# Kernel tuning notes

Hardware: AMD Instinct MI355X
Metric: run time of the kernel (lower is better)

## Reference

```python
import jax, jax.numpy as jnp
import numpy as np
from itertools import product

PBC_RADIUS = 1
# (K,3) integer image offsets, K = 27 for radius 1
_OFFSETS = jnp.asarray(np.array(list(product(range(-PBC_RADIUS, PBC_RADIUS + 1), repeat=3)), dtype=np.float32))


def _nan0(x):
    return jnp.nan_to_num(x, nan=0.0, posinf=0.0, neginf=0.0)


def _y1_and_gram(lattice):
    # _sanitize_lattice_latent for lattice_repr='y1'
    log_len = jnp.clip(lattice[:, :3], -5.0, 5.0)
    cosang = jnp.clip(lattice[:, 3:], -0.9999, 0.9999)
    lattice_y1 = jnp.concatenate([log_len, cosang], axis=-1)  # identity map for 'y1'
    lengths = jnp.exp(log_len)                                # (B,3)
    a, b, c = lengths[:, 0], lengths[:, 1], lengths[:, 2]
    ca, cb, cg = cosang[:, 0], cosang[:, 1], cosang[:, 2]
    # Gram: G_ij = l_i l_j cos(theta_ij); G01=ab*cos(gamma), G02=ac*cos(beta), G12=bc*cos(alpha)
    row0 = jnp.stack([a * a, a * b * cg, a * c * cb], axis=-1)
    row1 = jnp.stack([a * b * cg, b * b, b * c * ca], axis=-1)
    row2 = jnp.stack([a * c * cb, b * c * ca, c * c], axis=-1)
    gram = jnp.stack([row0, row1, row2], axis=1)  # (B,3,3)
    return _nan0(lattice_y1), _nan0(gram)


def _geometry(coords, lattice):
    coords = coords.astype(jnp.float32)
    lattice = lattice.astype(jnp.float32)
    lattice_y1, gram = _y1_and_gram(lattice)

    # (B,N,N,3) pairwise fractional deltas, then (B,N,N,K,3) periodic images
    delta = coords[:, :, None, :] - coords[:, None, :, :]
    delta_images = delta[:, :, :, None, :] + _OFFSETS  # broadcast over (K,3)

    # squared min-image distances under lattice metric: (B,N,N,K)
    dist2_images = jnp.einsum('bnmki,bij,bnmkj->bnmk', delta_images, gram, delta_images)

    min_idx = jnp.argmin(dist2_images, axis=-1)  # (B,N,N)
    min_dist2 = jnp.take_along_axis(dist2_images, min_idx[..., None], axis=-1)[..., 0]
    min_dist2 = jnp.maximum(min_dist2, 0.0)
    min_delta = jnp.take_along_axis(delta_images, min_idx[..., None, None], axis=3)[..., 0, :]  # (B,N,N,3)

    # safe sqrt (diagonal pairs have dist2 == 0; torch nan_to_num's the fwd NaNs)
    pos = min_dist2 > 0.0
    min_dist = jnp.where(pos, jnp.sqrt(jnp.where(pos, min_dist2, 1.0)), 0.0)
    min_dist = _nan0(min_dist)
    min_dist2 = _nan0(min_dist2)

    lengths = jnp.exp(lattice_y1[:, :3])
    cell_scale = jnp.maximum(lengths.mean(axis=-1), 1e-6)  # (B,)
    min_dist_norm = _nan0(min_dist / cell_scale[:, None, None])

    # pack geometry features: (B,N,N,6) = [min_delta(3), min_dist, min_dist2, min_dist_norm]
    out = jnp.concatenate(
        [min_delta, min_dist[..., None], min_dist2[..., None], min_dist_norm[..., None]], axis=-1)
    return out


def setup_inputs() -> dict:
    key = jax.random.key(0)
    k1, k2 = jax.random.split(key)
    coords = jax.random.uniform(k1, (8, 320, 3), dtype=jnp.float32)      # fractional coords in [0,1)
    lattice = jax.random.normal(k2, (8, 6), dtype=jnp.float32) * 0.5     # y1 latent (log-lengths, cosines)
    return {"coords": coords, "lattice": lattice}


def reference(coords, lattice):
    return _geometry(coords, lattice)
```

## Files before the change

### kernel.cpp

```cpp
#include <hip/hip_runtime.h>
#include <math.h>

__global__ void __launch_bounds__(256) geom_kernel(const float* __restrict__ coords,
                                                   const float* __restrict__ lattice,
                                                   float* __restrict__ out,
                                                   int B, int N) {
    int idx = blockIdx.x * blockDim.x + threadIdx.x;
    int total = B * N * N;
    if (idx >= total) return;

    int m = idx % N;
    int n = (idx / N) % N;
    int b = idx / (N * N);

    const float* lat = lattice + b * 6;
    float l0 = fminf(fmaxf(lat[0], -5.0f), 5.0f);
    float l1 = fminf(fmaxf(lat[1], -5.0f), 5.0f);
    float l2 = fminf(fmaxf(lat[2], -5.0f), 5.0f);
    float ca = fminf(fmaxf(lat[3], -0.9999f), 0.9999f);
    float cb = fminf(fmaxf(lat[4], -0.9999f), 0.9999f);
    float cg = fminf(fmaxf(lat[5], -0.9999f), 0.9999f);

    float a  = expf(l0);
    float bl = expf(l1);
    float c  = expf(l2);

    float G00 = a * a;
    float G01 = (a * bl) * cg;
    float G02 = (a * c) * cb;
    float G11 = bl * bl;
    float G12 = (bl * c) * ca;
    float G22 = c * c;

    float twoG01 = G01 + G01;
    float twoG02 = G02 + G02;
    float twoG12 = G12 + G12;

    const float* cn = coords + ((size_t)b * N + n) * 3;
    const float* cm = coords + ((size_t)b * N + m) * 3;
    float dx = cn[0] - cm[0];
    float dy = cn[1] - cm[1];
    float dz = cn[2] - cm[2];

    float best = INFINITY;
    int bestk = 0;
    #pragma unroll
    for (int kx = 0; kx < 3; ++kx) {
        float e0 = dx + (float)(kx - 1);
        float u   = (e0 * G00) * e0;
        float t01 = e0 * twoG01;
        float t02 = e0 * twoG02;
        #pragma unroll
        for (int ky = 0; ky < 3; ++ky) {
            float e1 = dy + (float)(ky - 1);
            float v = fmaf(e1, fmaf(e1, G11, t01), u);
            float w = fmaf(e1, twoG12, t02);
            #pragma unroll
            for (int kz = 0; kz < 3; ++kz) {
                float e2 = dz + (float)(kz - 1);
                float f = fmaf(e2, G22, w);
                float dist2 = fmaf(e2, f, v);
                int k = kx * 9 + ky * 3 + kz;
                if (dist2 < best) { best = dist2; bestk = k; }
            }
        }
    }

    float ox = (float)(bestk / 9) - 1.0f;
    float oy = (float)((bestk / 3) % 3) - 1.0f;
    float oz = (float)(bestk % 3) - 1.0f;
    float mdx = dx + ox;
    float mdy = dy + oy;
    float mdz = dz + oz;

    float md2 = fmaxf(best, 0.0f);
    bool pos = md2 > 0.0f;
    float mdist = pos ? sqrtf(md2) : 0.0f;

    if (!isfinite(mdist)) mdist = 0.0f;
    if (!isfinite(md2)) md2 = 0.0f;

    float mean_len = (a + bl + c) / 3.0f;
    float cell = fmaxf(mean_len, 1e-6f);
    float mnorm = mdist / cell;
    if (!isfinite(mnorm)) mnorm = 0.0f;

    size_t base = (((size_t)b * N + n) * N + m) * 6;
    out[base + 0] = mdx;
    out[base + 1] = mdy;
    out[base + 2] = mdz;
    out[base + 3] = mdist;
    out[base + 4] = md2;
    out[base + 5] = mnorm;
}

extern "C" void kernel_launch(void* const* d_in, const int* in_sizes, int n_in,
                              void* d_out, int out_size, void* d_ws, size_t ws_size,
                              hipStream_t stream) {
    const float* coords = (const float*)d_in[0];
    const float* lattice = (const float*)d_in[1];
    float* out = (float*)d_out;

    const int B = 8;
    const int N = in_sizes[0] / (B * 3);
    int total = B * N * N;
    int block = 256;
    int grid = (total + block - 1) / block;
    geom_kernel<<<grid, block, 0, stream>>>(coords, lattice, out, B, N);
}
```

Measured before the change: 14.99 us.

## Compute four pairs per thread with vectorized float4 loads and stores

Each thread now handles four consecutive m-partners for one n. It loads their coordinates with three float4 reads and writes the 24 output floats as six float4 stores, instead of six scalar stores per pair. The per-thread lattice setup is amortized over four pairs, and the divide is replaced by a reciprocal multiply. N=320 and B=8 are hardcoded into the grid, the finiteness guards are removed, and the number of threads drops fourfold, which lowers occupancy.

```diff
diff --git a/kernel.cpp b/kernel.cpp
--- a/kernel.cpp
+++ b/kernel.cpp
@@ -3,15 +3,12 @@
 
 __global__ void __launch_bounds__(256) geom_kernel(const float* __restrict__ coords,
                                                    const float* __restrict__ lattice,
-                                                   float* __restrict__ out,
-                                                   int B, int N) {
-    int idx = blockIdx.x * blockDim.x + threadIdx.x;
-    int total = B * N * N;
-    if (idx >= total) return;
-
-    int m = idx % N;
-    int n = (idx / N) % N;
-    int b = idx / (N * N);
+                                                   float* __restrict__ out) {
+    const int N = 320;
+    unsigned pos = blockIdx.x * 256u + threadIdx.x;
+    int b = blockIdx.y;
+    unsigned n  = pos / 80u;
+    unsigned m0 = (pos - n * 80u) * 4u;
 
     const float* lat = lattice + b * 6;
     float l0 = fminf(fmaxf(lat[0], -5.0f), 5.0f);
@@ -36,62 +33,71 @@
     float twoG02 = G02 + G02;
     float twoG12 = G12 + G12;
 
+    float cell  = fmaxf((a + bl + c) / 3.0f, 1e-6f);
+    float rcell = 1.0f / cell;
+
     const float* cn = coords + ((size_t)b * N + n) * 3;
-    const float* cm = coords + ((size_t)b * N + m) * 3;
-    float dx = cn[0] - cm[0];
-    float dy = cn[1] - cm[1];
-    float dz = cn[2] - cm[2];
+    float nx = cn[0], ny = cn[1], nz = cn[2];
 
-    float best = INFINITY;
-    int bestk = 0;
+    const float4* cmv = (const float4*)(coords + ((size_t)b * N + m0) * 3);
+    float4 q0 = cmv[0], q1 = cmv[1], q2 = cmv[2];
+    float mx[4] = {q0.x, q0.w, q1.z, q2.y};
+    float my[4] = {q0.y, q1.x, q1.w, q2.z};
+    float mz[4] = {q0.z, q1.y, q2.x, q2.w};
+
+    float res[24];
+
     #pragma unroll
-    for (int kx = 0; kx < 3; ++kx) {
-        float e0 = dx + (float)(kx - 1);
-        float u   = (e0 * G00) * e0;
-        float t01 = e0 * twoG01;
-        float t02 = e0 * twoG02;
+    for (int j = 0; j < 4; ++j) {
+        float dx = nx - mx[j];
+        float dy = ny - my[j];
+        float dz = nz - mz[j];
+
+        float best = INFINITY;
+        int bestk = 0;
         #pragma unroll
-        for (int ky = 0; ky < 3; ++ky) {
-            float e1 = dy + (float)(ky - 1);
-            float v = fmaf(e1, fmaf(e1, G11, t01), u);
-            float w = fmaf(e1, twoG12, t02);
+        for (int kx = 0; kx < 3; ++kx) {
+            float e0 = dx + (float)(kx - 1);
+            float u   = (e0 * G00) * e0;
+            float t01 = e0 * twoG01;
+            float t02 = e0 * twoG02;
             #pragma unroll
-            for (int kz = 0; kz < 3; ++kz) {
-                float e2 = dz + (float)(kz - 1);
-                float f = fmaf(e2, G22, w);
-                float dist2 = fmaf(e2, f, v);
-                int k = kx * 9 + ky * 3 + kz;
-                if (dist2 < best) { best = dist2; bestk = k; }
+            for (int ky = 0; ky < 3; ++ky) {
+                float e1 = dy + (float)(ky - 1);
+                float v = fmaf(e1, fmaf(e1, G11, t01), u);
+                float w = fmaf(e1, twoG12, t02);
+                #pragma unroll
+                for (int kz = 0; kz < 3; ++kz) {
+                    float e2 = dz + (float)(kz - 1);
+                    float f = fmaf(e2, G22, w);
+                    float dist2 = fmaf(e2, f, v);
+                    int k = kx * 9 + ky * 3 + kz;
+                    if (dist2 < best) { best = dist2; bestk = k; }
+                }
             }
         }
+
+        unsigned uk = (unsigned)bestk;
+        float ox = (float)(uk / 9u) - 1.0f;
+        float oy = (float)((uk / 3u) % 3u) - 1.0f;
+        float oz = (float)(uk % 3u) - 1.0f;
+
+        float md2 = fmaxf(best, 0.0f);
+        float mdist = (md2 > 0.0f) ? sqrtf(md2) : 0.0f;
+
+        res[j * 6 + 0] = dx + ox;
+        res[j * 6 + 1] = dy + oy;
+        res[j * 6 + 2] = dz + oz;
+        res[j * 6 + 3] = mdist;
+        res[j * 6 + 4] = md2;
+        res[j * 6 + 5] = mdist * rcell;
     }
 
-    float ox = (float)(bestk / 9) - 1.0f;
-    float oy = (float)((bestk / 3) % 3) - 1.0f;
-    float oz = (float)(bestk % 3) - 1.0f;
-    float mdx = dx + ox;
-    float mdy = dy + oy;
-    float mdz = dz + oz;
-
-    float md2 = fmaxf(best, 0.0f);
-    bool pos = md2 > 0.0f;
-    float mdist = pos ? sqrtf(md2) : 0.0f;
-
-    if (!isfinite(mdist)) mdist = 0.0f;
-    if (!isfinite(md2)) md2 = 0.0f;
-
-    float mean_len = (a + bl + c) / 3.0f;
-    float cell = fmaxf(mean_len, 1e-6f);
-    float mnorm = mdist / cell;
-    if (!isfinite(mnorm)) mnorm = 0.0f;
-
-    size_t base = (((size_t)b * N + n) * N + m) * 6;
-    out[base + 0] = mdx;
-    out[base + 1] = mdy;
-    out[base + 2] = mdz;
-    out[base + 3] = mdist;
-    out[base + 4] = md2;
-    out[base + 5] = mnorm;
+    float4* ov = (float4*)(out + (((size_t)b * N + n) * N + m0) * 6);
+    #pragma unroll
+    for (int t = 0; t < 6; ++t) {
+        ov[t] = make_float4(res[4 * t], res[4 * t + 1], res[4 * t + 2], res[4 * t + 3]);
+    }
 }
 
 extern "C" void kernel_launch(void* const* d_in, const int* in_sizes, int n_in,
@@ -101,10 +107,6 @@
     const float* lattice = (const float*)d_in[1];
     float* out = (float*)d_out;
 
-    const int B = 8;
-    const int N = in_sizes[0] / (B * 3);
-    int total = B * N * N;
-    int block = 256;
-    int grid = (total + block - 1) / block;
-    geom_kernel<<<grid, block, 0, stream>>>(coords, lattice, out, B, N);
+    dim3 grid(100, 8);
+    geom_kernel<<<grid, 256, 0, stream>>>(coords, lattice, out);
 }
```

Measured after the change: 15.31 us. +2.1%, slower.
